# Optimization experiments

Measured on AMD Instinct MI355X. Metric: run time of the kernel, lower is better.

The kernel has to match this reference:

```python
import jax, jax.numpy as jnp
import numpy as np

N_NODES = 50000
IN_DIM = 512
OUT_DIM = 128
N_EDGES = 1600000


def setup_inputs() -> dict:
    key = jax.random.key(0)
    k1, k2, k3, k4, k5 = jax.random.split(key, 5)
    x = jax.random.normal(k1, (N_NODES, IN_DIM), dtype=jnp.float32)
    weight = jax.random.normal(k2, (IN_DIM, OUT_DIM), dtype=jnp.float32)
    edge_row = jax.random.randint(k3, (N_EDGES,), 0, N_NODES, dtype=jnp.int32)
    edge_col = jax.random.randint(k4, (N_EDGES,), 0, N_NODES, dtype=jnp.int32)
    edge_val = jax.random.uniform(k5, (N_EDGES,), dtype=jnp.float32)
    return {"x": x, "weight": weight, "edge_row": edge_row,
            "edge_col": edge_col, "edge_val": edge_val}


def reference(x, weight, edge_row, edge_col, edge_val):
    # Dense feature transform: xw = x @ W   [N, OUT_DIM]
    xw = jnp.matmul(x, weight)
    # Sparse adjacency SpMM in COO form: out[r] += val * xw[c]
    msgs = edge_val[:, None] * xw[edge_col]          # [E, OUT_DIM]
    out = jax.ops.segment_sum(msgs, edge_row, num_segments=N_NODES)
    # activation=True, bias=False per init defaults
    return jax.nn.relu(out)
```

## Files before the change

### kernel.cpp

```cpp
#include <hip/hip_runtime.h>
#include <hip/hip_bf16.h>

#define N_NODES 50000
#define IN_DIM 512
#define OUT_DIM 128
#define N_EDGES 1600000

#define NPART 8
#define ROWS_PER_PART 6250
#define CAP 96

typedef __attribute__((ext_vector_type(8))) short short8;
typedef __attribute__((ext_vector_type(4))) float floatx4;
typedef __attribute__((ext_vector_type(2))) float floatx2;
typedef __attribute__((ext_vector_type(4))) uint uintx4;

__device__ __forceinline__ ushort f2bf(float f) {
    __hip_bfloat16 h = __float2bfloat16(f);
    return *reinterpret_cast<ushort*>(&h);
}

constexpr size_t OFF_XWB   = 0;
constexpr size_t OFF_WT    = 12800000;
constexpr size_t OFF_CUR_F = 12931072;
constexpr size_t OFF_SRT_F = 13131264;
constexpr size_t OFF_OFFS  = 12931072;
constexpr size_t OFF_CUR_S = 13131264;
constexpr size_t OFF_SRT_S = 13331456;

__global__ __launch_bounds__(256) void conv_wt(const float* __restrict__ w,
                                               ushort* __restrict__ wt) {
    int t = blockIdx.x * 256 + threadIdx.x;
    if (t < IN_DIM * OUT_DIM) {
        int k = t >> 7;
        int c = t & 127;
        wt[(size_t)c * IN_DIM + k] = f2bf(w[t]);
    }
}

__device__ __forceinline__ void gemm_tile_body(const float* __restrict__ x,
                                               const ushort* __restrict__ wt,
                                               ushort* __restrict__ xwb,
                                               int block_row, char* Alds, char* Blds,
                                               int tid) {
    const int w = tid >> 6;
    const int lane = tid & 63;

    floatx4 acc[8];
#pragma unroll
    for (int i = 0; i < 8; ++i) acc[i] = (floatx4){0.f, 0.f, 0.f, 0.f};

    for (int k0 = 0; k0 < IN_DIM; k0 += 64) {
#pragma unroll
        for (int it = 0; it < 4; ++it) {
            int f4 = tid + it * 256;
            int r = f4 >> 4;
            int f4c = f4 & 15;
            int grow = block_row + r;
            float4 v = make_float4(0.f, 0.f, 0.f, 0.f);
            if (grow < N_NODES)
                v = *reinterpret_cast<const float4*>(&x[(size_t)grow * IN_DIM + k0 + f4c * 4]);
            ushort4 b = make_ushort4(f2bf(v.x), f2bf(v.y), f2bf(v.z), f2bf(v.w));
            int off = r * 128 + ((f4c * 8) ^ ((r & 7) << 4));
            *reinterpret_cast<ushort4*>(Alds + off) = b;
        }
#pragma unroll
        for (int it = 0; it < 4; ++it) {
            int j = tid * 16 + it * 4096;
            int c = j >> 7;
            int inner = j & 127;
            ulonglong2 v = *reinterpret_cast<const ulonglong2*>(
                reinterpret_cast<const char*>(wt) + (size_t)c * 1024 + k0 * 2 + inner);
            int off = c * 128 + (inner ^ ((c & 7) << 4));
            *reinterpret_cast<ulonglong2*>(Blds + off) = v;
        }
        __syncthreads();

#pragma unroll
        for (int kb = 0; kb < 2; ++kb) {
            int ar = w * 16 + (lane & 15);
            int koffb = kb * 64 + (lane >> 4) * 16;
            short8 afrag = *reinterpret_cast<const short8*>(
                Alds + ar * 128 + (koffb ^ ((ar & 7) << 4)));
#pragma unroll
            for (int ct = 0; ct < 8; ++ct) {
                int bc = ct * 16 + (lane & 15);
                short8 bfrag = *reinterpret_cast<const short8*>(
                    Blds + bc * 128 + (koffb ^ ((bc & 7) << 4)));
                acc[ct] = __builtin_amdgcn_mfma_f32_16x16x32_bf16(afrag, bfrag, acc[ct], 0, 0, 0);
            }
        }
        __syncthreads();
    }

    const int orow0 = block_row + w * 16 + (lane >> 4) * 4;
    const int ocol = lane & 15;
#pragma unroll
    for (int ct = 0; ct < 8; ++ct) {
#pragma unroll
        for (int i = 0; i < 4; ++i) {
            int grow = orow0 + i;
            if (grow < N_NODES)
                xwb[(size_t)grow * OUT_DIM + ct * 16 + ocol] = f2bf(acc[ct][i]);
        }
    }
}

__global__ __launch_bounds__(256) void gemm_xw_mfma(const float* __restrict__ x,
                                                    const ushort* __restrict__ wt,
                                                    ushort* __restrict__ xwb) {
    __shared__ char lds[24576];
    gemm_tile_body(x, wt, xwb, blockIdx.x * 64, lds, lds + 8192, threadIdx.x);
}

__global__ __launch_bounds__(256) void build_cap4(const int* __restrict__ erow,
                                                  const int* __restrict__ ecol,
                                                  const float* __restrict__ eval_,
                                                  int* __restrict__ cur,
                                                  uint* __restrict__ srt) {
    const int part = blockIdx.x & (NPART - 1);
    const int sub = blockIdx.x >> 3;
    const int lo = part * ROWS_PER_PART;
    const int hi = lo + ROWS_PER_PART;
    for (int e = sub * 256 + threadIdx.x; e < N_EDGES; e += 65536) {
        int r = erow[e];
        if (r >= lo && r < hi) {
            int n = atomicAdd(&cur[r], 1);
            if (n < CAP) {
                srt[(size_t)r * CAP + n] = ((uint)f2bf(eval_[e]) << 16) | (uint)ecol[e];
            }
        }
    }
}

__global__ __launch_bounds__(256) void aggregate_cap4(const uint* __restrict__ srt,
                                                      const int* __restrict__ cur,
                                                      const ushort* __restrict__ xwb,
                                                      float* __restrict__ out) {
    int row = blockIdx.x * 4 + (threadIdx.x >> 6);
    if (row >= N_NODES) return;
    int lane = threadIdx.x & 63;
    int cnt = cur[row];
    if (cnt > CAP) cnt = CAP;
    const uint* seg = srt + (size_t)row * CAP;
    const uint* base = reinterpret_cast<const uint*>(xwb);

    float a0 = 0.f, a1 = 0.f, b0 = 0.f, b1 = 0.f;
    float c0 = 0.f, c1 = 0.f, d0 = 0.f, d1 = 0.f;
    int i = 0;
    for (; i + 3 < cnt; i += 4) {
        uintx4 p4 = __builtin_nontemporal_load(reinterpret_cast<const uintx4*>(&seg[i]));
        uint m0 = base[(size_t)(p4.x & 0xFFFFu) * 64 + lane];
        uint m1 = base[(size_t)(p4.y & 0xFFFFu) * 64 + lane];
        uint m2 = base[(size_t)(p4.z & 0xFFFFu) * 64 + lane];
        uint m3 = base[(size_t)(p4.w & 0xFFFFu) * 64 + lane];
        float v0 = __uint_as_float(p4.x & 0xFFFF0000u);
        float v1 = __uint_as_float(p4.y & 0xFFFF0000u);
        float v2 = __uint_as_float(p4.z & 0xFFFF0000u);
        float v3 = __uint_as_float(p4.w & 0xFFFF0000u);
        a0 = fmaf(v0, __uint_as_float(m0 << 16), a0);
        a1 = fmaf(v0, __uint_as_float(m0 & 0xFFFF0000u), a1);
        b0 = fmaf(v1, __uint_as_float(m1 << 16), b0);
        b1 = fmaf(v1, __uint_as_float(m1 & 0xFFFF0000u), b1);
        c0 = fmaf(v2, __uint_as_float(m2 << 16), c0);
        c1 = fmaf(v2, __uint_as_float(m2 & 0xFFFF0000u), c1);
        d0 = fmaf(v3, __uint_as_float(m3 << 16), d0);
        d1 = fmaf(v3, __uint_as_float(m3 & 0xFFFF0000u), d1);
    }
    for (; i < cnt; ++i) {
        uint pk = seg[i];
        uint m = base[(size_t)(pk & 0xFFFFu) * 64 + lane];
        float v = __uint_as_float(pk & 0xFFFF0000u);
        a0 = fmaf(v, __uint_as_float(m << 16), a0);
        a1 = fmaf(v, __uint_as_float(m & 0xFFFF0000u), a1);
    }
    float s0 = (a0 + b0) + (c0 + d0);
    float s1 = (a1 + b1) + (c1 + d1);
    floatx2 r = {fmaxf(s0, 0.f), fmaxf(s1, 0.f)};
    __builtin_nontemporal_store(r, reinterpret_cast<floatx2*>(&out[(size_t)row * OUT_DIM + lane * 2]));
}

__global__ __launch_bounds__(256) void hist_part(const int* __restrict__ erow,
                                                 int* __restrict__ cnt) {
    const int part = blockIdx.x & (NPART - 1);
    const int sub = blockIdx.x >> 3;
    const int lo = part * ROWS_PER_PART;
    const int hi = lo + ROWS_PER_PART;
    for (int e = sub * 256 + threadIdx.x; e < N_EDGES; e += 65536) {
        int r = erow[e];
        if (r >= lo && r < hi) atomicAdd(&cnt[r], 1);
    }
}

__global__ __launch_bounds__(1024) void scan_offsets(int* __restrict__ offs) {
    __shared__ int partials[1024];
    const int tid = threadIdx.x;
    const int CHUNK = (N_NODES + 1023) / 1024;
    int begin = 1 + tid * CHUNK;
    int end = begin + CHUNK;
    if (end > N_NODES + 1) end = N_NODES + 1;

    int sum = 0;
    for (int i = begin; i < end; ++i) sum += offs[i];
    partials[tid] = sum;
    __syncthreads();
    for (int d = 1; d < 1024; d <<= 1) {
        int v = (tid >= d) ? partials[tid - d] : 0;
        __syncthreads();
        partials[tid] += v;
        __syncthreads();
    }
    int run = (tid == 0) ? 0 : partials[tid - 1];
    for (int i = begin; i < end; ++i) {
        run += offs[i];
        offs[i] = run;
    }
}

__global__ __launch_bounds__(256) void build_part(const int* __restrict__ erow,
                                                  const int* __restrict__ ecol,
                                                  const float* __restrict__ eval_,
                                                  const int* __restrict__ offs,
                                                  int* __restrict__ cur,
                                                  int2* __restrict__ srt) {
    const int part = blockIdx.x & (NPART - 1);
    const int sub = blockIdx.x >> 3;
    const int lo = part * ROWS_PER_PART;
    const int hi = lo + ROWS_PER_PART;
    for (int e = sub * 256 + threadIdx.x; e < N_EDGES; e += 65536) {
        int r = erow[e];
        if (r >= lo && r < hi) {
            int pos = offs[r] + atomicAdd(&cur[r], 1);
            srt[pos] = make_int2(ecol[e], __float_as_int(eval_[e]));
        }
    }
}

__global__ __launch_bounds__(256) void aggregate_rows(const int2* __restrict__ srt,
                                                      const int* __restrict__ offs,
                                                      const ushort* __restrict__ xwb,
                                                      float* __restrict__ out) {
    int row = blockIdx.x * 4 + (threadIdx.x >> 6);
    if (row >= N_NODES) return;
    int lane = threadIdx.x & 63;
    int start = offs[row];
    int end = offs[row + 1];
    const uint* base = reinterpret_cast<const uint*>(xwb);

    float a0 = 0.f, a1 = 0.f;
    for (int i = start; i < end; ++i) {
        int2 p = srt[i];
        uint m = base[(size_t)p.x * 64 + lane];
        float v = __int_as_float(p.y);
        a0 = fmaf(v, __uint_as_float(m << 16), a0);
        a1 = fmaf(v, __uint_as_float(m & 0xFFFF0000u), a1);
    }
    float2 r = make_float2(fmaxf(a0, 0.f), fmaxf(a1, 0.f));
    *reinterpret_cast<float2*>(&out[(size_t)row * OUT_DIM + lane * 2]) = r;
}

extern "C" void kernel_launch(void* const* d_in, const int* in_sizes, int n_in,
                              void* d_out, int out_size, void* d_ws, size_t ws_size,
                              hipStream_t stream) {
    const float* x     = (const float*)d_in[0];
    const float* w     = (const float*)d_in[1];
    const int*   erow  = (const int*)d_in[2];
    const int*   ecol  = (const int*)d_in[3];
    const float* eval_ = (const float*)d_in[4];
    float* out = (float*)d_out;

    char* ws = (char*)d_ws;
    ushort* xwb = (ushort*)(ws + OFF_XWB);
    ushort* wt  = (ushort*)(ws + OFF_WT);

    conv_wt<<<(IN_DIM * OUT_DIM + 255) / 256, 256, 0, stream>>>(w, wt);

    const size_t need_fast = OFF_SRT_F + (size_t)N_NODES * CAP * sizeof(uint);
    if (ws_size >= need_fast) {
        int*  cur = (int*)(ws + OFF_CUR_F);
        uint* srt = (uint*)(ws + OFF_SRT_F);
        (void)hipMemsetAsync(ws + OFF_CUR_F, 0, (size_t)N_NODES * sizeof(int), stream);
        build_cap4<<<2048, 256, 0, stream>>>(erow, ecol, eval_, cur, srt);
        gemm_xw_mfma<<<(N_NODES + 63) / 64, 256, 0, stream>>>(x, wt, xwb);
        aggregate_cap4<<<(N_NODES + 3) / 4, 256, 0, stream>>>(srt, cur, xwb, out);
    } else {
        int*  offs = (int*)(ws + OFF_OFFS);
        int*  cur  = (int*)(ws + OFF_CUR_S);
        int2* srt  = (int2*)(ws + OFF_SRT_S);
        (void)hipMemsetAsync(ws + OFF_OFFS, 0, OFF_SRT_S - OFF_OFFS, stream);
        hist_part<<<2048, 256, 0, stream>>>(erow, offs + 1);
        scan_offsets<<<1, 1024, 0, stream>>>(offs);
        gemm_xw_mfma<<<(N_NODES + 63) / 64, 256, 0, stream>>>(x, wt, xwb);
        build_part<<<2048, 256, 0, stream>>>(erow, ecol, eval_, offs, cur, srt);
        aggregate_rows<<<(N_NODES + 3) / 4, 256, 0, stream>>>(srt, offs, xwb, out);
    }
}
```

Baseline: 180.0 us.

## Load GEMM fragments directly from global memory and split edge build into two phases

The GEMM no longer stages tiles of x and W through LDS. Each lane now loads its MFMA A and B fragments straight from global memory, which removes the LDS stores and both __syncthreads per k-step. W is small and should stay resident in cache, but each lane's x row read now strides across rows and is less coalesced. Separately, the edge build kernel now scans the edge list twice, each pass covering half of its partition's row range. This aims to shrink the scattered write and atomic footprint per pass, at the cost of reading erow twice.

```diff
diff --git a/kernel.cpp b/kernel.cpp
--- a/kernel.cpp
+++ b/kernel.cpp
@@ -8,6 +8,7 @@
 
 #define NPART 8
 #define ROWS_PER_PART 6250
+#define HALF_RANGE 3125
 #define CAP 96
 
 typedef __attribute__((ext_vector_type(8))) short short8;
@@ -38,59 +39,42 @@
     }
 }
 
-__device__ __forceinline__ void gemm_tile_body(const float* __restrict__ x,
-                                               const ushort* __restrict__ wt,
-                                               ushort* __restrict__ xwb,
-                                               int block_row, char* Alds, char* Blds,
-                                               int tid) {
+__global__ __launch_bounds__(256) void gemm_direct(const float* __restrict__ x,
+                                                   const ushort* __restrict__ wt,
+                                                   ushort* __restrict__ xwb) {
+    const int tid = threadIdx.x;
     const int w = tid >> 6;
     const int lane = tid & 63;
+    const int block_row = blockIdx.x * 64;
+
+    const int ar = block_row + w * 16 + (lane & 15);
+    const int arow = (ar < N_NODES) ? ar : (N_NODES - 1);
+    const float* xrow = x + (size_t)arow * IN_DIM;
+    const int g8 = (lane >> 4) * 8;
 
     floatx4 acc[8];
 #pragma unroll
     for (int i = 0; i < 8; ++i) acc[i] = (floatx4){0.f, 0.f, 0.f, 0.f};
 
-    for (int k0 = 0; k0 < IN_DIM; k0 += 64) {
-#pragma unroll
-        for (int it = 0; it < 4; ++it) {
-            int f4 = tid + it * 256;
-            int r = f4 >> 4;
-            int f4c = f4 & 15;
-            int grow = block_row + r;
-            float4 v = make_float4(0.f, 0.f, 0.f, 0.f);
-            if (grow < N_NODES)
-                v = *reinterpret_cast<const float4*>(&x[(size_t)grow * IN_DIM + k0 + f4c * 4]);
-            ushort4 b = make_ushort4(f2bf(v.x), f2bf(v.y), f2bf(v.z), f2bf(v.w));
-            int off = r * 128 + ((f4c * 8) ^ ((r & 7) << 4));
-            *reinterpret_cast<ushort4*>(Alds + off) = b;
-        }
-#pragma unroll
-        for (int it = 0; it < 4; ++it) {
-            int j = tid * 16 + it * 4096;
-            int c = j >> 7;
-            int inner = j & 127;
-            ulonglong2 v = *reinterpret_cast<const ulonglong2*>(
-                reinterpret_cast<const char*>(wt) + (size_t)c * 1024 + k0 * 2 + inner);
-            int off = c * 128 + (inner ^ ((c & 7) << 4));
-            *reinterpret_cast<ulonglong2*>(Blds + off) = v;
-        }
-        __syncthreads();
-
-#pragma unroll
-        for (int kb = 0; kb < 2; ++kb) {
-            int ar = w * 16 + (lane & 15);
-            int koffb = kb * 64 + (lane >> 4) * 16;
-            short8 afrag = *reinterpret_cast<const short8*>(
-                Alds + ar * 128 + (koffb ^ ((ar & 7) << 4)));
-#pragma unroll
-            for (int ct = 0; ct < 8; ++ct) {
-                int bc = ct * 16 + (lane & 15);
-                short8 bfrag = *reinterpret_cast<const short8*>(
-                    Blds + bc * 128 + (koffb ^ ((bc & 7) << 4)));
-                acc[ct] = __builtin_amdgcn_mfma_f32_16x16x32_bf16(afrag, bfrag, acc[ct], 0, 0, 0);
-            }
-        }
-        __syncthreads();
+    const ushort* brow[8];
+#pragma unroll
+    for (int ct = 0; ct < 8; ++ct)
+        brow[ct] = wt + (size_t)(ct * 16 + (lane & 15)) * IN_DIM;
+
+    for (int k0 = 0; k0 < IN_DIM; k0 += 32) {
+        const int kk = k0 + g8;
+        float4 af0 = *reinterpret_cast<const float4*>(xrow + kk);
+        float4 af1 = *reinterpret_cast<const float4*>(xrow + kk + 4);
+        short8 afrag;
+        afrag[0] = (short)f2bf(af0.x); afrag[1] = (short)f2bf(af0.y);
+        afrag[2] = (short)f2bf(af0.z); afrag[3] = (short)f2bf(af0.w);
+        afrag[4] = (short)f2bf(af1.x); afrag[5] = (short)f2bf(af1.y);
+        afrag[6] = (short)f2bf(af1.z); afrag[7] = (short)f2bf(af1.w);
+#pragma unroll
+        for (int ct = 0; ct < 8; ++ct) {
+            short8 bfrag = *reinterpret_cast<const short8*>(brow[ct] + kk);
+            acc[ct] = __builtin_amdgcn_mfma_f32_16x16x32_bf16(afrag, bfrag, acc[ct], 0, 0, 0);
+        }
     }
 
     const int orow0 = block_row + w * 16 + (lane >> 4) * 4;
@@ -104,13 +88,6 @@
                 xwb[(size_t)grow * OUT_DIM + ct * 16 + ocol] = f2bf(acc[ct][i]);
         }
     }
-}
-
-__global__ __launch_bounds__(256) void gemm_xw_mfma(const float* __restrict__ x,
-                                                    const ushort* __restrict__ wt,
-                                                    ushort* __restrict__ xwb) {
-    __shared__ char lds[24576];
-    gemm_tile_body(x, wt, xwb, blockIdx.x * 64, lds, lds + 8192, threadIdx.x);
 }
 
 __global__ __launch_bounds__(256) void build_cap4(const int* __restrict__ erow,
@@ -120,14 +97,17 @@
                                                   uint* __restrict__ srt) {
     const int part = blockIdx.x & (NPART - 1);
     const int sub = blockIdx.x >> 3;
-    const int lo = part * ROWS_PER_PART;
-    const int hi = lo + ROWS_PER_PART;
-    for (int e = sub * 256 + threadIdx.x; e < N_EDGES; e += 65536) {
-        int r = erow[e];
-        if (r >= lo && r < hi) {
-            int n = atomicAdd(&cur[r], 1);
-            if (n < CAP) {
-                srt[(size_t)r * CAP + n] = ((uint)f2bf(eval_[e]) << 16) | (uint)ecol[e];
+#pragma unroll
+    for (int phase = 0; phase < 2; ++phase) {
+        const int lo = part * ROWS_PER_PART + phase * HALF_RANGE;
+        const int hi = lo + HALF_RANGE;
+        for (int e = sub * 256 + threadIdx.x; e < N_EDGES; e += 65536) {
+            int r = erow[e];
+            if (r >= lo && r < hi) {
+                int n = atomicAdd(&cur[r], 1);
+                if (n < CAP) {
+                    srt[(size_t)r * CAP + n] = ((uint)f2bf(eval_[e]) << 16) | (uint)ecol[e];
+                }
             }
         }
     }
@@ -281,7 +261,7 @@
         uint* srt = (uint*)(ws + OFF_SRT_F);
         (void)hipMemsetAsync(ws + OFF_CUR_F, 0, (size_t)N_NODES * sizeof(int), stream);
         build_cap4<<<2048, 256, 0, stream>>>(erow, ecol, eval_, cur, srt);
-        gemm_xw_mfma<<<(N_NODES + 63) / 64, 256, 0, stream>>>(x, wt, xwb);
+        gemm_direct<<<(N_NODES + 63) / 64, 256, 0, stream>>>(x, wt, xwb);
         aggregate_cap4<<<(N_NODES + 3) / 4, 256, 0, stream>>>(srt, cur, xwb, out);
     } else {
         int*  offs = (int*)(ws + OFF_OFFS);
@@ -290,7 +270,7 @@
         (void)hipMemsetAsync(ws + OFF_OFFS, 0, OFF_SRT_S - OFF_OFFS, stream);
         hist_part<<<2048, 256, 0, stream>>>(erow, offs + 1);
         scan_offsets<<<1, 1024, 0, stream>>>(offs);
-        gemm_xw_mfma<<<(N_NODES + 63) / 64, 256, 0, stream>>>(x, wt, xwb);
+        gemm_direct<<<(N_NODES + 63) / 64, 256, 0, stream>>>(x, wt, xwb);
         build_part<<<2048, 256, 0, stream>>>(erow, ecol, eval_, offs, cur, srt);
         aggregate_rows<<<(N_NODES + 3) / 4, 256, 0, stream>>>(srt, offs, xwb, out);
     }
```

Measured after the change: 261.2 us. 45.1% more time.

## Prefetch next K-slice of x and W into registers during MFMA compute

Applied to the files above, without the earlier changes.

The GEMM kernel now issues global loads for the next 64-wide K slice of x and the transposed weight into registers right after the LDS barrier, so their latency overlaps the MFMA work on the current slice. Index math is hoisted out of the loop and out-of-range rows are clamped to row 0 instead of branching. Launch bounds add a minimum of 4 blocks per CU, and the helper function is inlined into the kernel with separate LDS arrays. The cost is more live registers for the prefetch buffers and one redundant wraparound load on the final iteration.

```diff
diff --git a/kernel.cpp b/kernel.cpp
--- a/kernel.cpp
+++ b/kernel.cpp
@@ -38,43 +38,72 @@
     }
 }
 
-__device__ __forceinline__ void gemm_tile_body(const float* __restrict__ x,
-                                               const ushort* __restrict__ wt,
-                                               ushort* __restrict__ xwb,
-                                               int block_row, char* Alds, char* Blds,
-                                               int tid) {
+__global__ __launch_bounds__(256, 4) void gemm_xw_mfma(const float* __restrict__ x,
+                                                       const ushort* __restrict__ wt,
+                                                       ushort* __restrict__ xwb) {
+    __shared__ char Alds[8192];
+    __shared__ char Blds[16384];
+    const int tid = threadIdx.x;
     const int w = tid >> 6;
     const int lane = tid & 63;
+    const int block_row = blockIdx.x * 64;
 
     floatx4 acc[8];
 #pragma unroll
     for (int i = 0; i < 8; ++i) acc[i] = (floatx4){0.f, 0.f, 0.f, 0.f};
 
+    int a_r[4], a_c[4], b_c[4], b_i[4];
+#pragma unroll
+    for (int it = 0; it < 4; ++it) {
+        int f4 = tid + it * 256;
+        a_r[it] = f4 >> 4;
+        a_c[it] = (f4 & 15) * 4;
+        int j = tid * 16 + it * 4096;
+        b_c[it] = j >> 7;
+        b_i[it] = j & 127;
+    }
+
+    float4 va[4];
+    ulonglong2 vb[4];
+
+#pragma unroll
+    for (int it = 0; it < 4; ++it) {
+        int grow = block_row + a_r[it];
+        int rr = (grow < N_NODES) ? grow : 0;
+        va[it] = *reinterpret_cast<const float4*>(&x[(size_t)rr * IN_DIM + a_c[it]]);
+    }
+#pragma unroll
+    for (int it = 0; it < 4; ++it)
+        vb[it] = *reinterpret_cast<const ulonglong2*>(
+            reinterpret_cast<const char*>(wt) + (size_t)b_c[it] * 1024 + b_i[it]);
+
     for (int k0 = 0; k0 < IN_DIM; k0 += 64) {
 #pragma unroll
         for (int it = 0; it < 4; ++it) {
-            int f4 = tid + it * 256;
-            int r = f4 >> 4;
-            int f4c = f4 & 15;
-            int grow = block_row + r;
-            float4 v = make_float4(0.f, 0.f, 0.f, 0.f);
-            if (grow < N_NODES)
-                v = *reinterpret_cast<const float4*>(&x[(size_t)grow * IN_DIM + k0 + f4c * 4]);
-            ushort4 b = make_ushort4(f2bf(v.x), f2bf(v.y), f2bf(v.z), f2bf(v.w));
-            int off = r * 128 + ((f4c * 8) ^ ((r & 7) << 4));
+            ushort4 b = make_ushort4(f2bf(va[it].x), f2bf(va[it].y),
+                                     f2bf(va[it].z), f2bf(va[it].w));
+            int off = a_r[it] * 128 + ((a_c[it] * 2) ^ ((a_r[it] & 7) << 4));
             *reinterpret_cast<ushort4*>(Alds + off) = b;
         }
 #pragma unroll
         for (int it = 0; it < 4; ++it) {
-            int j = tid * 16 + it * 4096;
-            int c = j >> 7;
-            int inner = j & 127;
-            ulonglong2 v = *reinterpret_cast<const ulonglong2*>(
-                reinterpret_cast<const char*>(wt) + (size_t)c * 1024 + k0 * 2 + inner);
-            int off = c * 128 + (inner ^ ((c & 7) << 4));
-            *reinterpret_cast<ulonglong2*>(Blds + off) = v;
+            int off = b_c[it] * 128 + (b_i[it] ^ ((b_c[it] & 7) << 4));
+            *reinterpret_cast<ulonglong2*>(Blds + off) = vb[it];
         }
         __syncthreads();
+
+        const int kn = (k0 + 64) & (IN_DIM - 1);
+#pragma unroll
+        for (int it = 0; it < 4; ++it) {
+            int grow = block_row + a_r[it];
+            int rr = (grow < N_NODES) ? grow : 0;
+            va[it] = *reinterpret_cast<const float4*>(
+                &x[(size_t)rr * IN_DIM + kn + a_c[it]]);
+        }
+#pragma unroll
+        for (int it = 0; it < 4; ++it)
+            vb[it] = *reinterpret_cast<const ulonglong2*>(
+                reinterpret_cast<const char*>(wt) + (size_t)b_c[it] * 1024 + kn * 2 + b_i[it]);
 
 #pragma unroll
         for (int kb = 0; kb < 2; ++kb) {
@@ -104,13 +133,6 @@
                 xwb[(size_t)grow * OUT_DIM + ct * 16 + ocol] = f2bf(acc[ct][i]);
         }
     }
-}
-
-__global__ __launch_bounds__(256) void gemm_xw_mfma(const float* __restrict__ x,
-                                                    const ushort* __restrict__ wt,
-                                                    ushort* __restrict__ xwb) {
-    __shared__ char lds[24576];
-    gemm_tile_body(x, wt, xwb, blockIdx.x * 64, lds, lds + 8192, threadIdx.x);
 }
 
 __global__ __launch_bounds__(256) void build_cap4(const int* __restrict__ erow,
```

New measurement: 206.9 us. +14.9%, slower.
